# Kernel optimization log

Hardware: AMD Instinct MI355X
Metric: run time of the kernel (lower is better)

The kernel has to match this reference:

```python
import jax, jax.numpy as jnp
import numpy as np

B, S, EMB = 2048, 512, 64
CARD = [2, 2, 2, 11, 19, 31, 34]  # gender, korean, primary, job, place, add, rep


def setup_inputs() -> dict:
    key = jax.random.key(0)
    ks = jax.random.split(key, 24)
    cont_x = jax.random.normal(ks[0], (B, S, 5), dtype=jnp.float32)
    cols = [jax.random.randint(ks[1 + i], (B, S, 1), 0, c) for i, c in enumerate(CARD)]
    cat_x = jnp.concatenate(cols, axis=2).astype(jnp.int32)  # [B,S,7]
    length = jax.random.randint(ks[8], (B,), 1, S + 1).astype(jnp.int32)  # valid lengths >= 1
    inp = {"cont_x": cont_x, "cat_x": cat_x, "length": length}
    for i, c in enumerate(CARD):
        inp[f"emb{i}"] = jax.random.normal(ks[9 + i], (c, EMB), dtype=jnp.float32) * 0.02
    inp["W_cont"] = jax.random.normal(ks[16], (5, EMB), dtype=jnp.float32) * (1.0 / np.sqrt(5.0))
    inp["b_cont"] = jnp.zeros((EMB,), dtype=jnp.float32)
    inp["W1"] = jax.random.normal(ks[17], (128, 64), dtype=jnp.float32) * (1.0 / np.sqrt(128.0))
    inp["b1"] = jnp.zeros((64,), dtype=jnp.float32)
    inp["W2"] = jax.random.normal(ks[18], (64, 2), dtype=jnp.float32) * (1.0 / np.sqrt(64.0))
    inp["b2"] = jnp.zeros((2,), dtype=jnp.float32)
    return inp


def reference(cont_x, cat_x, length, emb0, emb1, emb2, emb3, emb4, emb5, emb6,
              W_cont, b_cont, W1, b1, W2, b2):
    tables = (emb0, emb1, emb2, emb3, emb4, emb5, emb6)
    # mean of 7 per-column embedding lookups -> [B,S,EMB]
    cat_embs = sum(t[cat_x[:, :, i]] for i, t in enumerate(tables)) / 7.0
    cont_h = jax.nn.relu(cont_x @ W_cont + b_cont)  # [B,S,EMB]
    x = jnp.concatenate([cat_embs, cont_h], axis=2)  # [B,S,128]
    # fused masked segment-mean over valid prefix (replaces per-sample host loop)
    mask = (jnp.arange(x.shape[1])[None, :] < length[:, None]).astype(x.dtype)  # [B,S]
    pooled = jnp.einsum('bsd,bs->bd', x, mask) / length[:, None].astype(x.dtype)
    h = jax.nn.relu(pooled @ W1 + b1)
    out = jax.nn.relu(h @ W2 + b2)  # dropout p=0.0 -> identity
    return out
```

## Files before the change

### kernel.cpp

```cpp
#include <hip/hip_runtime.h>
#include <hip/hip_bf16.h>


#define CARD3 11
#define CARD4 19
#define CARD5 31
#define CARD6 34

typedef __attribute__((ext_vector_type(8))) short bf16x8;
typedef __attribute__((ext_vector_type(4))) float f32x4;
typedef __attribute__((ext_vector_type(4))) unsigned uintx4;
typedef int   int4a  __attribute__((ext_vector_type(4), aligned(4)));
typedef int   int2a  __attribute__((ext_vector_type(2), aligned(4)));
typedef float flt4a  __attribute__((ext_vector_type(4), aligned(4)));

static __device__ __forceinline__ unsigned pk_bf16(float a, float b) {
    unsigned ua = __float_as_uint(a), ub = __float_as_uint(b);
    ua += 0x7FFFu + ((ua >> 16) & 1u);
    ub += 0x7FFFu + ((ub >> 16) & 1u);
    return ((ua >> 16) & 0xFFFFu) | (ub & 0xFFFF0000u);
}

static __device__ __forceinline__ float rdlane(float v, int i) {
    return __builtin_bit_cast(float,
        __builtin_amdgcn_readlane(__builtin_bit_cast(int, v), i));
}

__global__ __launch_bounds__(64) void mlp_wave(
    const float* __restrict__ cont_x,
    const int*   __restrict__ cat_x,
    const int*   __restrict__ length,
    const float* __restrict__ e0, const float* __restrict__ e1,
    const float* __restrict__ e2, const float* __restrict__ e3,
    const float* __restrict__ e4, const float* __restrict__ e5,
    const float* __restrict__ e6,
    const float* __restrict__ W_cont,
    const float* __restrict__ b_cont,
    const float* __restrict__ W1,
    const float* __restrict__ b1,
    const float* __restrict__ W2,
    const float* __restrict__ b2,
    float*       __restrict__ out,
    int S)
{
    constexpr int HOFF[4] = {0, 11, 30, 61};
    constexpr int CARD[7] = {2, 2, 2, CARD3, CARD4, CARD5, CARD6};
    constexpr int OFFB[7] = {0, 2, 4, 6, 17, 36, 67};

    __shared__ int   hist[96];
    __shared__ float pcontl[64];
    __shared__ float pls[136];

    const int b    = blockIdx.x;
    const int l    = threadIdx.x;
    const int lo16 = l & 15;
    const bool lo  = (l < 16);

    const int len = length[b];
    const int nt  = (len + 63) >> 6;

    hist[l] = 0;
    if (l < 32) hist[64 + l] = 0;

    const int*   cat7  = cat_x  + (size_t)b * S * 7;
    const float* cont5 = cont_x + (size_t)b * S * 5;

    unsigned q0, q1, q2;
    {
        const float w0 = W_cont[l],        w1 = W_cont[64 + l];
        const float w2 = W_cont[128 + l],  w3 = W_cont[192 + l];
        const float w4 = W_cont[256 + l],  w5 = b_cont[l];
        q0 = pk_bf16(w0, w1); q1 = pk_bf16(w2, w3); q2 = pk_bf16(w4, w5);
    }
    bf16x8 Bf[4];
#pragma unroll
    for (int ntc = 0; ntc < 4; ++ntc) {
        const int src = ntc * 16 + lo16;
        unsigned c0 = (unsigned)__shfl((int)q0, src);
        unsigned c1 = (unsigned)__shfl((int)q1, src);
        unsigned c2 = (unsigned)__shfl((int)q2, src);
        c0 = lo ? c0 : 0u; c1 = lo ? c1 : 0u; c2 = lo ? c2 : 0u;
        const uintx4 bu = {c0, c1, c2, 0u};
        Bf[ntc] = __builtin_bit_cast(bf16x8, bu);
    }

    int   c1pack = 0;
    f32x4 sum0 = {0.f, 0.f, 0.f, 0.f};
    f32x4 sum1 = sum0, sum2 = sum0, sum3 = sum0;
    const f32x4 z = {0.f, 0.f, 0.f, 0.f};

    int4a caA = {0,0,0,0}, caB = {0,0,0,0};
    int2a cbA = {0,0},     cbB = {0,0};
    int   ccA = 0,         ccB = 0;
    flt4a xaA = {0,0,0,0}, xaB = {0,0,0,0};
    float xbA = 0.f,       xbB = 0.f;

#define LOADA(T) do { const int* cp_ = cat7 + (size_t)((T)*64 + l) * 7;          \
        caA = *(const int4a*)cp_; cbA = *(const int2a*)(cp_ + 4); ccA = cp_[6];  \
        const float* xp_ = cont5 + (size_t)((T)*64 + l) * 5;                     \
        xaA = *(const flt4a*)xp_; xbA = xp_[4]; } while (0)
#define LOADB(T) do { const int* cp_ = cat7 + (size_t)((T)*64 + l) * 7;          \
        caB = *(const int4a*)cp_; cbB = *(const int2a*)(cp_ + 4); ccB = cp_[6];  \
        const float* xp_ = cont5 + (size_t)((T)*64 + l) * 5;                     \
        xaB = *(const flt4a*)xp_; xbB = xp_[4]; } while (0)

    auto COMPUTE = [&](int base, const int4a& ca, const int2a& cb, int cc,
                       const flt4a& xa, float xb) {
        const bool valid = (base + l < len);
        float x0 = 0.f, x1 = 0.f, x2 = 0.f, x3 = 0.f, x4 = 0.f;
        if (valid) {
            c1pack += ca.x + (ca.y << 10) + (ca.z << 20);
            atomicAdd(&hist[HOFF[0] + ca.w], 1);
            atomicAdd(&hist[HOFF[1] + cb.x], 1);
            atomicAdd(&hist[HOFF[2] + cb.y], 1);
            atomicAdd(&hist[HOFF[3] + cc],   1);
            x0 = xa.x; x1 = xa.y; x2 = xa.z; x3 = xa.w; x4 = xb;
        }
        const float aug = valid ? 1.0f : 0.0f;
        const unsigned p0 = pk_bf16(x0, x1);
        const unsigned p1 = pk_bf16(x2, x3);
        const unsigned p2 = pk_bf16(x4, aug);

#pragma unroll
        for (int t4 = 0; t4 < 4; ++t4) {
            const int src = t4 * 16 + lo16;
            unsigned a0 = (unsigned)__shfl((int)p0, src);
            unsigned a1 = (unsigned)__shfl((int)p1, src);
            unsigned a2 = (unsigned)__shfl((int)p2, src);
            a0 = lo ? a0 : 0u; a1 = lo ? a1 : 0u; a2 = lo ? a2 : 0u;
            const uintx4 au = {a0, a1, a2, 0u};
            const bf16x8 Af = __builtin_bit_cast(bf16x8, au);

            const f32x4 d0 = __builtin_amdgcn_mfma_f32_16x16x32_bf16(Af, Bf[0], z, 0, 0, 0);
            const f32x4 d1 = __builtin_amdgcn_mfma_f32_16x16x32_bf16(Af, Bf[1], z, 0, 0, 0);
            const f32x4 d2 = __builtin_amdgcn_mfma_f32_16x16x32_bf16(Af, Bf[2], z, 0, 0, 0);
            const f32x4 d3 = __builtin_amdgcn_mfma_f32_16x16x32_bf16(Af, Bf[3], z, 0, 0, 0);
#pragma unroll
            for (int i = 0; i < 4; ++i) {
                sum0[i] += fmaxf(d0[i], 0.f);
                sum1[i] += fmaxf(d1[i], 0.f);
                sum2[i] += fmaxf(d2[i], 0.f);
                sum3[i] += fmaxf(d3[i], 0.f);
            }
        }
    };

    LOADA(0);
    if (nt > 1) LOADB(1);
#pragma unroll 1
    for (int t = 0; t < nt; t += 2) {
        COMPUTE(t * 64, caA, cbA, ccA, xaA, xbA);
        if (t + 2 < nt) LOADA(t + 2);
        if (t + 1 < nt) {
            COMPUTE((t + 1) * 64, caB, cbB, ccB, xaB, xbB);
            if (t + 3 < nt) LOADB(t + 3);
        }
    }
#undef LOADA
#undef LOADB

#pragma unroll
    for (int off = 1; off <= 32; off <<= 1) c1pack += __shfl_xor(c1pack, off);

    float s0 = sum0[0] + sum0[1] + sum0[2] + sum0[3];
    float s1 = sum1[0] + sum1[1] + sum1[2] + sum1[3];
    float s2 = sum2[0] + sum2[1] + sum2[2] + sum2[3];
    float s3 = sum3[0] + sum3[1] + sum3[2] + sum3[3];
    s0 += __shfl_xor(s0, 16); s0 += __shfl_xor(s0, 32);
    s1 += __shfl_xor(s1, 16); s1 += __shfl_xor(s1, 32);
    s2 += __shfl_xor(s2, 16); s2 += __shfl_xor(s2, 32);
    s3 += __shfl_xor(s3, 16); s3 += __shfl_xor(s3, 32);
    if (lo) {
        pcontl[lo16]      = s0;
        pcontl[16 + lo16] = s1;
        pcontl[32 + lo16] = s2;
        pcontl[48 + lo16] = s3;
    }

    const float inv_len = 1.0f / (float)len;
    const float inv7    = inv_len * (1.0f / 7.0f);

    {
        const int d = 64 + l;
        pls[d + (d >> 5)] = pcontl[l] * inv_len;
    }

    float wA, wB;
    {
        const int j  = l >> 1;
        const int c1 = (c1pack >> (10 * j)) & 0x3FF;
        const float bw = (l & 1) ? (float)c1 : (float)(len - c1);
        wA = (l < 6) ? bw * inv7 : (float)hist[l - 6] * inv7;
        wB = (l < 37) ? (float)hist[58 + l] * inv7 : 0.f;
    }

    float pa0 = 0.f, pa1 = 0.f, pa2 = 0.f, pa3 = 0.f;
    {
        int cnt = 0;
#pragma unroll
        for (int t = 0; t < 7; ++t) {
            const float* tab = (t == 0) ? e0 : (t == 1) ? e1 : (t == 2) ? e2
                             : (t == 3) ? e3 : (t == 4) ? e4 : (t == 5) ? e5 : e6;
#pragma unroll
            for (int v = 0; v < CARD[t]; ++v) {
                const int i = OFFB[t] + v;
                const float f = (i < 64) ? rdlane(wA, i) : rdlane(wB, i - 64);
                const float ev = tab[v * 64 + l];
                if ((cnt & 3) == 0)      pa0 = fmaf(f, ev, pa0);
                else if ((cnt & 3) == 1) pa1 = fmaf(f, ev, pa1);
                else if ((cnt & 3) == 2) pa2 = fmaf(f, ev, pa2);
                else                     pa3 = fmaf(f, ev, pa3);
                ++cnt;
            }
        }
    }
    pls[l + (l >> 5)] = (pa0 + pa1) + (pa2 + pa3);

    const int qg = lo16;
    const int sl = l >> 4;
    float hb0, hb1, hb2, hb3;
    {
        const flt4a b14 = *(const flt4a*)(b1 + 4 * qg);
        const bool iss0 = (sl == 0);
        hb0 = iss0 ? b14.x : 0.f;
        hb1 = iss0 ? b14.y : 0.f;
        hb2 = iss0 ? b14.z : 0.f;
        hb3 = iss0 ? b14.w : 0.f;
    }
#pragma unroll
    for (int i = 0; i < 32; ++i) {
        const int d = sl * 32 + i;
        const float f = pls[d + sl];
        const flt4a wv = *(const flt4a*)(W1 + d * 64 + 4 * qg);
        hb0 = fmaf(f, wv.x, hb0);
        hb1 = fmaf(f, wv.y, hb1);
        hb2 = fmaf(f, wv.z, hb2);
        hb3 = fmaf(f, wv.w, hb3);
    }
    hb0 += __shfl_xor(hb0, 16); hb0 += __shfl_xor(hb0, 32);
    hb1 += __shfl_xor(hb1, 16); hb1 += __shfl_xor(hb1, 32);
    hb2 += __shfl_xor(hb2, 16); hb2 += __shfl_xor(hb2, 32);
    hb3 += __shfl_xor(hb3, 16); hb3 += __shfl_xor(hb3, 32);
    const float h0 = fmaxf(hb0, 0.f);
    const float h1 = fmaxf(hb1, 0.f);
    const float h2 = fmaxf(hb2, 0.f);
    const float h3 = fmaxf(hb3, 0.f);

    const flt4a w2a = *(const flt4a*)(W2 + 8 * qg);
    const flt4a w2b = *(const flt4a*)(W2 + 8 * qg + 4);
    float rr0 = h0 * w2a.x + h1 * w2a.z + h2 * w2b.x + h3 * w2b.z;
    float rr1 = h0 * w2a.y + h1 * w2a.w + h2 * w2b.y + h3 * w2b.w;
#pragma unroll
    for (int off = 1; off <= 8; off <<= 1) {
        rr0 += __shfl_xor(rr0, off);
        rr1 += __shfl_xor(rr1, off);
    }
    if (l == 0) {
        const float2 bb2 = *(const float2*)b2;
        float2 res;
        res.x = fmaxf(rr0 + bb2.x, 0.f);
        res.y = fmaxf(rr1 + bb2.y, 0.f);
        ((float2*)out)[b] = res;
    }
}

extern "C" void kernel_launch(void* const* d_in, const int* in_sizes, int n_in,
                              void* d_out, int out_size, void* d_ws, size_t ws_size,
                              hipStream_t stream)
{
    const float* cont_x = (const float*)d_in[0];
    const int*   cat_x  = (const int*)d_in[1];
    const int*   length = (const int*)d_in[2];
    const float* e0     = (const float*)d_in[3];
    const float* e1     = (const float*)d_in[4];
    const float* e2     = (const float*)d_in[5];
    const float* e3     = (const float*)d_in[6];
    const float* e4     = (const float*)d_in[7];
    const float* e5     = (const float*)d_in[8];
    const float* e6     = (const float*)d_in[9];
    const float* W_cont = (const float*)d_in[10];
    const float* b_cont = (const float*)d_in[11];
    const float* W1     = (const float*)d_in[12];
    const float* b1     = (const float*)d_in[13];
    const float* W2     = (const float*)d_in[14];
    const float* b2     = (const float*)d_in[15];
    float*       out    = (float*)d_out;

    const int B = in_sizes[2];
    const int S = in_sizes[0] / (B * 5);

    hipLaunchKernelGGL(mlp_wave, dim3(B), dim3(64), 0, stream,
                       cont_x, cat_x, length,
                       e0, e1, e2, e3, e4, e5, e6,
                       W_cont, b_cont, W1, b1, W2, b2,
                       out, S);
}
```

Before: 18.51 us.

## Issue all eight sequence-tile loads upfront before compute

Replaces the double-buffered loop over sequence tiles with eight fully unrolled tile loads issued at kernel start, right after reading the length, followed by guarded compute per tile. All memory requests go out at once, so load latency stops being serialized across iterations. This hardcodes S=512 (eight tiles of 64) and loads every tile even when the length is short, which adds bandwidth and register pressure. launch_bounds gains a min-blocks hint of 2.

```diff
diff --git a/kernel.cpp b/kernel.cpp
--- a/kernel.cpp
+++ b/kernel.cpp
@@ -26,7 +26,7 @@
         __builtin_amdgcn_readlane(__builtin_bit_cast(int, v), i));
 }
 
-__global__ __launch_bounds__(64) void mlp_wave(
+__global__ __launch_bounds__(64, 2) void mlp_wave(
     const float* __restrict__ cont_x,
     const int*   __restrict__ cat_x,
     const int*   __restrict__ length,
@@ -57,13 +57,28 @@
     const bool lo  = (l < 16);
 
     const int len = length[b];
-    const int nt  = (len + 63) >> 6;
+
+    const int*   cat7  = cat_x  + (size_t)b * S * 7;
+    const float* cont5 = cont_x + (size_t)b * S * 5;
+
+#define DECL_TILE(N) int4a ca##N; int2a cb##N; int cc##N; flt4a xa##N; float xb##N;
+#define LOAD_TILE(N) do {                                                         \
+        const int* cp_ = cat7 + (size_t)((N) * 64 + l) * 7;                       \
+        ca##N = *(const int4a*)cp_; cb##N = *(const int2a*)(cp_ + 4);             \
+        cc##N = cp_[6];                                                           \
+        const float* xp_ = cont5 + (size_t)((N) * 64 + l) * 5;                    \
+        xa##N = *(const flt4a*)xp_; xb##N = xp_[4]; } while (0)
+
+    DECL_TILE(0) DECL_TILE(1) DECL_TILE(2) DECL_TILE(3)
+    DECL_TILE(4) DECL_TILE(5) DECL_TILE(6) DECL_TILE(7)
+    LOAD_TILE(0); LOAD_TILE(1); LOAD_TILE(2); LOAD_TILE(3);
+    LOAD_TILE(4); LOAD_TILE(5); LOAD_TILE(6); LOAD_TILE(7);
+#undef LOAD_TILE
+
+    const int nt = (len + 63) >> 6;
 
     hist[l] = 0;
     if (l < 32) hist[64 + l] = 0;
-
-    const int*   cat7  = cat_x  + (size_t)b * S * 7;
-    const float* cont5 = cont_x + (size_t)b * S * 5;
 
     unsigned q0, q1, q2;
     {
@@ -88,21 +103,6 @@
     f32x4 sum0 = {0.f, 0.f, 0.f, 0.f};
     f32x4 sum1 = sum0, sum2 = sum0, sum3 = sum0;
     const f32x4 z = {0.f, 0.f, 0.f, 0.f};
-
-    int4a caA = {0,0,0,0}, caB = {0,0,0,0};
-    int2a cbA = {0,0},     cbB = {0,0};
-    int   ccA = 0,         ccB = 0;
-    flt4a xaA = {0,0,0,0}, xaB = {0,0,0,0};
-    float xbA = 0.f,       xbB = 0.f;
-
-#define LOADA(T) do { const int* cp_ = cat7 + (size_t)((T)*64 + l) * 7;          \
-        caA = *(const int4a*)cp_; cbA = *(const int2a*)(cp_ + 4); ccA = cp_[6];  \
-        const float* xp_ = cont5 + (size_t)((T)*64 + l) * 5;                     \
-        xaA = *(const flt4a*)xp_; xbA = xp_[4]; } while (0)
-#define LOADB(T) do { const int* cp_ = cat7 + (size_t)((T)*64 + l) * 7;          \
-        caB = *(const int4a*)cp_; cbB = *(const int2a*)(cp_ + 4); ccB = cp_[6];  \
-        const float* xp_ = cont5 + (size_t)((T)*64 + l) * 5;                     \
-        xaB = *(const flt4a*)xp_; xbB = xp_[4]; } while (0)
 
     auto COMPUTE = [&](int base, const int4a& ca, const int2a& cb, int cc,
                        const flt4a& xa, float xb) {
@@ -145,19 +145,15 @@
         }
     };
 
-    LOADA(0);
-    if (nt > 1) LOADB(1);
-#pragma unroll 1
-    for (int t = 0; t < nt; t += 2) {
-        COMPUTE(t * 64, caA, cbA, ccA, xaA, xbA);
-        if (t + 2 < nt) LOADA(t + 2);
-        if (t + 1 < nt) {
-            COMPUTE((t + 1) * 64, caB, cbB, ccB, xaB, xbB);
-            if (t + 3 < nt) LOADB(t + 3);
-        }
-    }
-#undef LOADA
-#undef LOADB
+    COMPUTE(0, ca0, cb0, cc0, xa0, xb0);
+    if (nt > 1) COMPUTE(64,  ca1, cb1, cc1, xa1, xb1);
+    if (nt > 2) COMPUTE(128, ca2, cb2, cc2, xa2, xb2);
+    if (nt > 3) COMPUTE(192, ca3, cb3, cc3, xa3, xb3);
+    if (nt > 4) COMPUTE(256, ca4, cb4, cc4, xa4, xb4);
+    if (nt > 5) COMPUTE(320, ca5, cb5, cc5, xa5, xb5);
+    if (nt > 6) COMPUTE(384, ca6, cb6, cc6, xa6, xb6);
+    if (nt > 7) COMPUTE(448, ca7, cb7, cc7, xa7, xb7);
+#undef DECL_TILE
 
 #pragma unroll
     for (int off = 1; off <= 32; off <<= 1) c1pack += __shfl_xor(c1pack, off);
```

After: 22.37 us. 1.21x slower.
